# Performance work log

Measured on AMD Instinct MI355X. Metric: run time of the kernel, lower is better.

The kernel has to match this reference:

```python
import jax, jax.numpy as jnp
import numpy as np

N, E, IN, OUT = 50000, 1600000, 64, 64
DIM, K = 2, 5          # pseudo-coordinate dim, kernel size per dim
KP = K ** DIM          # 25 kernel weight matrices
S = 2 ** DIM           # 4 non-zero linear B-spline basis products per edge
# bit pattern per basis product: bits[s, d] in {0,1}
_BITS = np.array([[(s >> d) & 1 for d in range(DIM)] for s in range(S)], dtype=np.int32)
_OFFS = np.array([K ** (DIM - 1 - d) for d in range(DIM)], dtype=np.int32)  # row-major flatten


def setup_inputs() -> dict:
    key = jax.random.key(0)
    ks = jax.random.split(key, 6)
    x = jax.random.normal(ks[0], (N, IN), dtype=jnp.float32)
    edge_index = jax.random.randint(ks[1], (2, E), 0, N)
    pseudo = jax.random.uniform(ks[2], (E, DIM), dtype=jnp.float32)
    bnd = 1.0 / np.sqrt(KP * IN)  # matches uniform(size) init in reset_parameters
    weight = jax.random.uniform(ks[3], (KP, IN, OUT), dtype=jnp.float32, minval=-bnd, maxval=bnd)
    root_weight = jax.random.uniform(ks[4], (IN, OUT), dtype=jnp.float32, minval=-bnd, maxval=bnd)
    bias = jax.random.uniform(ks[5], (OUT,), dtype=jnp.float32, minval=-bnd, maxval=bnd)
    return {"x": x, "edge_index": edge_index, "pseudo": pseudo,
            "weight": weight, "root_weight": root_weight, "bias": bias}


def _basis_and_index(pseudo):
    # open B-spline, degree 1: scale by (K - 1)
    v = pseudo * jnp.asarray(K - 1, pseudo.dtype)          # [E, DIM]
    lo = jnp.floor(v)
    frac = v - lo                                          # [E, DIM]
    lo = lo.astype(jnp.int32)
    bits = jnp.asarray(_BITS)                              # [S, DIM]
    # basis[e, s] = prod_d (frac if bit else 1-frac)
    terms = jnp.where(bits[None].astype(bool), frac[:, None, :], 1.0 - frac[:, None, :])
    basis = jnp.prod(terms, axis=-1)                       # [E, S]
    idx_d = (lo[:, None, :] + bits[None]) % K              # [E, S, DIM]; wrap is harmless (basis=0 there)
    idx = jnp.sum(idx_d * jnp.asarray(_OFFS), axis=-1)     # [E, S] flat weight index in [0, KP)
    return basis, idx


def reference(x, edge_index, pseudo, weight, root_weight, bias):
    row, col = edge_index[0], edge_index[1]                # row = target, col = source
    basis, idx = _basis_and_index(pseudo)                  # [E,S], [E,S]
    x_src = x[col]                                         # [E, IN] gather
    # Accumulate basis-weighted source features per (target node, kernel index),
    # then apply the dense [KP, IN, OUT] weights once (same math, no [E,IN,OUT] blowup).
    acc = jnp.zeros((N * KP, IN), x.dtype)
    for s in range(S):  # S=4, fixed structural loop
        acc = acc + jax.ops.segment_sum(basis[:, s:s + 1] * x_src,
                                        row * KP + idx[:, s], num_segments=N * KP)
    out = jnp.einsum('nki,kio->no', acc.reshape(N, KP, IN), weight)  # [N, OUT]
    deg = jax.ops.segment_sum(jnp.ones((E,), x.dtype), row, num_segments=N)
    out = out / jnp.clip(deg, 1.0)[:, None]                # mean over neighbors (1/N(i))
    return out + x @ root_weight + bias
```

## Files before the change

kernel.cpp:

```cpp
#include <hip/hip_runtime.h>
#include <hip/hip_fp16.h>
#include <hip/hip_bf16.h>


#define NN    50000
#define EE    1600000
#define NPB   16
#define KD    1664
#define ASTB  1672

#define NB    391
#define NSH   4
#define CCAP  1280
#define CSTR  16

#define REC_B 6250
#define XB_B  1563
#define WT_B  104

typedef unsigned short ushort_t;
typedef __attribute__((ext_vector_type(8))) short short8;
typedef __attribute__((ext_vector_type(4))) float f32x4;

static __device__ __forceinline__ ushort_t f2bf(float f) {
  union { float f; unsigned u; } v; v.f = f;
  return (ushort_t)((v.u + 0x7fffu + ((v.u >> 16) & 1u)) >> 16);
}
static __device__ __forceinline__ unsigned pk2bf(float a, float b) {
  __hip_bfloat162 h = __float22bfloat162_rn(make_float2(a, b));
  union { __hip_bfloat162 h; unsigned u; } cv; cv.h = h; return cv.u;
}
union S8 { short8 s; unsigned u[4]; };

__global__ __launch_bounds__(256) void k_prep(
    const int* __restrict__ ei, const float* __restrict__ pseudo,
    int* __restrict__ ccur, uint2* __restrict__ coarse,
    const float* __restrict__ x, ushort_t* __restrict__ xb,
    const float* __restrict__ w, const float* __restrict__ root,
    ushort_t* __restrict__ wt, int useXB) {
  const int b = blockIdx.x;
  const int tid = threadIdx.x;
  if (b < REC_B) {
    int e = b * 256 + tid;
    int row = ei[e], col = ei[EE + e];
    float2 pv = ((const float2*)pseudo)[e];
    float v0 = pv.x * 4.0f, v1 = pv.y * 4.0f;
    unsigned h0 = __half_as_ushort(__float2half(v0));
    unsigned h1 = __half_as_ushort(__float2half(v1));
    int c4 = (row >> 7) * NSH + (tid & (NSH - 1));
    int slot = atomicAdd(&ccur[c4 * CSTR], 1);
    if (slot < CCAP)
      coarse[(size_t)c4 * CCAP + slot] =
          make_uint2((unsigned)col | ((unsigned)(row & 127) << 16), h0 | (h1 << 16));
  } else if (b < REC_B + XB_B) {
    if (!useXB) return;
    int t = (b - REC_B) * 256 + tid;
    if (t < NN * 8) {
      const float4* xp = (const float4*)x + (size_t)t * 2;
      float4 aa = xp[0], bb = xp[1];
      S8 o;
      o.u[0] = pk2bf(aa.x, aa.y); o.u[1] = pk2bf(aa.z, aa.w);
      o.u[2] = pk2bf(bb.x, bb.y); o.u[3] = pk2bf(bb.z, bb.w);
      ((short8*)xb)[t] = o.s;
    }
  } else {
    int t = (b - REC_B - XB_B) * 256 + tid;
    int idx = t * 4;
    if (idx < 64 * KD) {
      int o = idx / KD, k = idx - o * KD;
#pragma unroll
      for (int q = 0; q < 4; ++q) {
        int kk = k + q;
        int kp = kk >> 6, c = kk & 63;
        int fi = 4 * (c & 15) + (c >> 4);
        wt[idx + q] = (kp < 25) ? f2bf(w[(kp * 64 + fi) * 64 + o])
                                : f2bf(root[fi * 64 + o]);
      }
    }
  }
}

__global__ __launch_bounds__(256) void k_sort(
    const int* __restrict__ ccur, const uint2* __restrict__ coarse,
    uint2* __restrict__ recs, uint2* __restrict__ nfo) {
  __shared__ int cnt[128], lpos[128], scn[128], red[256];
  const int c = blockIdx.x, tid = threadIdx.x;
  if (tid < 128) cnt[tid] = 0;
  const int pc = c * NSH;
  int a = 0;
  for (int i = tid; i < pc; i += 256) a += min(ccur[i * CSTR], CCAP);
  red[tid] = a;
  __syncthreads();
  for (int s = 128; s > 0; s >>= 1) { if (tid < s) red[tid] += red[tid + s]; __syncthreads(); }
  const int base = red[0];
  for (int s = 0; s < NSH; ++s) {
    int n = min(ccur[(pc + s) * CSTR], CCAP);
    const uint2* seg = coarse + (size_t)(pc + s) * CCAP;
    for (int i = tid; i < n; i += 256) atomicAdd(&cnt[(seg[i].x >> 16) & 127], 1);
  }
  __syncthreads();
  if (tid < 128) scn[tid] = cnt[tid];
  __syncthreads();
  for (int ofs = 1; ofs < 128; ofs <<= 1) {
    int v = 0;
    if (tid < 128 && tid >= ofs) v = scn[tid - ofs];
    __syncthreads();
    if (tid < 128 && tid >= ofs) scn[tid] += v;
    __syncthreads();
  }
  if (tid < 128) {
    int excl = scn[tid] - cnt[tid];
    lpos[tid] = base + excl;
    int row = c * 128 + tid;
    if (row < NN) nfo[row] = make_uint2((unsigned)(base + excl), (unsigned)cnt[tid]);
  }
  __syncthreads();
  for (int s = 0; s < NSH; ++s) {
    int n = min(ccur[(pc + s) * CSTR], CCAP);
    const uint2* seg = coarse + (size_t)(pc + s) * CCAP;
    for (int i = tid; i < n; i += 256) {
      uint2 r = seg[i];
      int dst = atomicAdd(&lpos[(r.x >> 16) & 127], 1);
      recs[dst] = make_uint2(r.x & 0xFFFFu, r.y);
    }
  }
}

template <bool XBF>
static __device__ __forceinline__ void do_chunk(
    const uint2 (&rq)[8], int kb, int m, int quad, int m15,
    float r0f, float c0f, float r1f, float c1f,
    const ushort_t* __restrict__ xb, const float* __restrict__ x,
    f32x4 (&acc)[2][4]) {
  unsigned cj[8], pj[8];
#pragma unroll
  for (int j = 0; j < 8; ++j) {
    cj[j] = min(rq[j].x, (unsigned)(NN - 1));
    pj[j] = rq[j].y;
  }
  uint2 g[8];
  float gf[4][8];
  if (XBF) {
#pragma unroll
    for (int j = 0; j < 8; ++j)
      g[j] = *(const uint2*)(xb + ((size_t)cj[j] << 6) + (m15 << 2));
  } else {
#pragma unroll
    for (int j = 0; j < 8; ++j) {
      float4 v = *(const float4*)(x + ((size_t)cj[j] << 6) + (m15 << 2));
      gf[0][j] = v.x; gf[1][j] = v.y; gf[2][j] = v.z; gf[3][j] = v.w;
    }
  }
  S8 aT0, aT1, bT[4];
#pragma unroll
  for (int p = 0; p < 4; ++p) {
    float a0[2], a1[2];
#pragma unroll
    for (int q = 0; q < 2; ++q) {
      int j = 2 * p + q;
      unsigned pv = pj[j];
      float v0 = __half2float(__ushort_as_half((ushort_t)(pv & 0xFFFFu)));
      float v1 = __half2float(__ushort_as_half((ushort_t)(pv >> 16)));
      bool ok = (kb + quad * 8 + j) < m;
      float p0 = fmaxf(0.f, 1.f - fabsf(v0 - r0f)) * fmaxf(0.f, 1.f - fabsf(v1 - c0f));
      float p1 = fmaxf(0.f, 1.f - fabsf(v0 - r1f)) * fmaxf(0.f, 1.f - fabsf(v1 - c1f));
      a0[q] = ok ? p0 : 0.0f;
      a1[q] = ok ? p1 : 0.0f;
    }
    aT0.u[p] = pk2bf(a0[0], a0[1]);
    aT1.u[p] = pk2bf(a1[0], a1[1]);
  }
  if (XBF) {
#pragma unroll
    for (int p = 0; p < 4; ++p) {
      bT[0].u[p] = (g[2 * p].x & 0xFFFFu) | (g[2 * p + 1].x << 16);
      bT[1].u[p] = (g[2 * p].x >> 16)     | (g[2 * p + 1].x & 0xFFFF0000u);
      bT[2].u[p] = (g[2 * p].y & 0xFFFFu) | (g[2 * p + 1].y << 16);
      bT[3].u[p] = (g[2 * p].y >> 16)     | (g[2 * p + 1].y & 0xFFFF0000u);
    }
  } else {
#pragma unroll
    for (int p = 0; p < 4; ++p)
#pragma unroll
      for (int t = 0; t < 4; ++t)
        bT[t].u[p] = pk2bf(gf[t][2 * p], gf[t][2 * p + 1]);
  }
  __builtin_amdgcn_s_setprio(1);
#pragma unroll
  for (int t = 0; t < 4; ++t) {
    acc[0][t] = __builtin_amdgcn_mfma_f32_16x16x32_bf16(aT0.s, bT[t].s, acc[0][t], 0, 0, 0);
    acc[1][t] = __builtin_amdgcn_mfma_f32_16x16x32_bf16(aT1.s, bT[t].s, acc[1][t], 0, 0, 0);
  }
  __builtin_amdgcn_s_setprio(0);
}

template <bool XBF>
__global__ __launch_bounds__(512, 4) void k_main(
    const uint2* __restrict__ recs, const uint2* __restrict__ nfo,
    const float* __restrict__ x, const ushort_t* __restrict__ xb,
    const ushort_t* __restrict__ wt, const float* __restrict__ bias,
    float* __restrict__ out) {
  __shared__ ushort_t accS[NPB * ASTB];
  __shared__ float    outp[2 * NPB * 64];
  __shared__ float    sinv[NPB];
  const int tid = threadIdx.x;
  const int lane = tid & 63;
  const int w = tid >> 6;
  const int nb = blockIdx.x * NPB;

  const int m15 = lane & 15, quad = lane >> 4;
  const float r0f = (float)(m15 / 5),        c0f = (float)(m15 % 5);
  const float r1f = (float)((16 + m15) / 5), c1f = (float)((16 + m15) % 5);
  const int fl = 4 * (lane & 15) + (lane >> 4);

#pragma unroll
  for (int nd = 0; nd < 2; ++nd) {
    const int row = (w << 1) + nd;
    const int node = nb + row;
    const uint2 nf = nfo[node];
    const int m = (int)nf.y;
    const float dcf = (float)max(m, 1);
    if (lane == 0) sinv[row] = 1.0f / dcf;
    accS[row * ASTB + 1600 + lane] = f2bf(x[(size_t)node * 64 + fl] * dcf);

    f32x4 acc[2][4];
#pragma unroll
    for (int a = 0; a < 2; ++a)
#pragma unroll
      for (int b = 0; b < 4; ++b) acc[a][b] = (f32x4){0.f, 0.f, 0.f, 0.f};

    const uint2* bket = recs + nf.x;
    for (int e0 = 0; e0 < m; e0 += 32) {
      uint2 rq[8];
#pragma unroll
      for (int j = 0; j < 8; ++j) rq[j] = bket[e0 + quad * 8 + j];
      do_chunk<XBF>(rq, e0, m, quad, m15, r0f, c0f, r1f, c1f, xb, x, acc);
    }

#pragma unroll
    for (int mt = 0; mt < 2; ++mt)
#pragma unroll
      for (int r = 0; r < 4; ++r) {
        int kp = mt * 16 + quad * 4 + r;
        if (kp < 25) {
#pragma unroll
          for (int nt = 0; nt < 4; ++nt)
            accS[row * ASTB + kp * 64 + nt * 16 + m15] = f2bf(acc[mt][nt][r]);
        }
      }
  }
  __syncthreads();

  {
    const int ntile = w & 3, kh = w >> 2;
    const int m2 = lane & 15, quad2 = lane >> 4;
    const int nn2 = ntile * 16 + m2;
    f32x4 d = {0.0f, 0.0f, 0.0f, 0.0f};
    const ushort_t* ab = &accS[m2 * ASTB + kh * 832 + quad2 * 8];
    const ushort_t* wb = &wt[(size_t)nn2 * KD + kh * 832 + quad2 * 8];
    short8 bfs[6];
#pragma unroll
    for (int kk = 0; kk < 6; ++kk) bfs[kk] = *(const short8*)(wb + kk * 32);
#pragma unroll
    for (int kk = 0; kk < 26; ++kk) {
      short8 af = *(const short8*)(ab + kk * 32);
      d = __builtin_amdgcn_mfma_f32_16x16x32_bf16(af, bfs[kk % 6], d, 0, 0, 0);
      if (kk + 6 < 26) bfs[kk % 6] = *(const short8*)(wb + (kk + 6) * 32);
    }
#pragma unroll
    for (int r = 0; r < 4; ++r)
      outp[kh * (NPB * 64) + (quad2 * 4 + r) * 64 + ntile * 16 + m2] = d[r];
  }
  __syncthreads();

  {
#pragma unroll
    for (int h = 0; h < 2; ++h) {
      int i = h * 512 + tid;
      int nl = i >> 6, o = i & 63;
      float conv = outp[i] + outp[NPB * 64 + i];
      out[(size_t)(nb + nl) * 64 + o] = conv * sinv[nl] + bias[o];
    }
  }
}

__global__ void k_sentinel(float* __restrict__ out) {
  int i = blockIdx.x * 256 + threadIdx.x;
  if (i < NN * 64) out[i] = 1000.0f;
}

extern "C" void kernel_launch(void* const* d_in, const int* in_sizes, int n_in,
                              void* d_out, int out_size, void* d_ws, size_t ws_size,
                              hipStream_t stream) {
  const float* x      = (const float*)d_in[0];
  const int*   ei     = (const int*)d_in[1];
  const float* pseudo = (const float*)d_in[2];
  const float* w      = (const float*)d_in[3];
  const float* root   = (const float*)d_in[4];
  const float* bias   = (const float*)d_in[5];
  float* out = (float*)d_out;
  (void)in_sizes; (void)n_in; (void)out_size;

  char* ws = (char*)d_ws;
  size_t off = 0;
  auto alloc = [&](size_t bytes) { size_t r = off; off += (bytes + 511) & ~(size_t)511; return r; };
  ushort_t* wt     = (ushort_t*)(ws + alloc((size_t)64 * KD * 2));
  int*      ccur   = (int*)(ws + alloc((size_t)NB * NSH * CSTR * 4));
  uint2*    nfo    = (uint2*)(ws + alloc((size_t)NN * 8));
  uint2*    recs   = (uint2*)(ws + alloc((size_t)EE * 8));
  uint2*    coarse = (uint2*)(ws + alloc((size_t)NB * NSH * CCAP * 8));
  size_t baseNeed  = off;
  ushort_t* xb     = (ushort_t*)(ws + alloc((size_t)NN * 64 * 2));
  size_t fullNeed  = off;

  if (ws_size < baseNeed) {
    k_sentinel<<<(NN * 64 + 255) / 256, 256, 0, stream>>>(out);
    return;
  }
  const int useXB = (ws_size >= fullNeed) ? 1 : 0;

  hipMemsetAsync(ccur, 0, (size_t)NB * NSH * CSTR * 4, stream);
  k_prep<<<REC_B + XB_B + WT_B, 256, 0, stream>>>(ei, pseudo, ccur, coarse,
                                                  x, xb, w, root, wt, useXB);
  k_sort<<<NB, 256, 0, stream>>>(ccur, coarse, recs, nfo);
  if (useXB)
    k_main<true><<<NN / NPB, 512, 0, stream>>>(recs, nfo, x, xb, wt, bias, out);
  else
    k_main<false><<<NN / NPB, 512, 0, stream>>>(recs, nfo, x, xb, wt, bias, out);
}
```

Baseline: 316.1 us.

## Split each node's feature columns across two waves with 1024-thread blocks

Doubles the block size to 1024 threads so each node's edge aggregation is handled by two waves. Each wave owns half of the 64 output feature columns, gathering 4-byte slices instead of 8-byte ones and issuing half as many MFMAs per chunk. The aim is more parallelism and less register pressure per wave, which helps hide gather latency. The cost is that every edge record and its basis weights are now loaded and computed twice, once per wave, and the dense second stage leaves half the waves idle.

```diff
diff --git a/kernel.cpp b/kernel.cpp
--- a/kernel.cpp
+++ b/kernel.cpp
@@ -128,37 +128,33 @@
 
 template <bool XBF>
 static __device__ __forceinline__ void do_chunk(
-    const uint2 (&rq)[8], int kb, int m, int quad, int m15,
+    const uint2 (&rq)[8], int kb, int m, int quad, int m15, int p,
     float r0f, float c0f, float r1f, float c1f,
     const ushort_t* __restrict__ xb, const float* __restrict__ x,
-    f32x4 (&acc)[2][4]) {
-  unsigned cj[8], pj[8];
-#pragma unroll
-  for (int j = 0; j < 8; ++j) {
-    cj[j] = min(rq[j].x, (unsigned)(NN - 1));
-    pj[j] = rq[j].y;
-  }
-  uint2 g[8];
-  float gf[4][8];
+    f32x4 (&acc)[2][2]) {
+  unsigned g[8];
+  float2 gf[8];
   if (XBF) {
 #pragma unroll
-    for (int j = 0; j < 8; ++j)
-      g[j] = *(const uint2*)(xb + ((size_t)cj[j] << 6) + (m15 << 2));
+    for (int j = 0; j < 8; ++j) {
+      unsigned c = min(rq[j].x, (unsigned)(NN - 1));
+      g[j] = *(const unsigned*)(xb + ((size_t)c << 6) + (m15 << 2) + (p << 1));
+    }
   } else {
 #pragma unroll
     for (int j = 0; j < 8; ++j) {
-      float4 v = *(const float4*)(x + ((size_t)cj[j] << 6) + (m15 << 2));
-      gf[0][j] = v.x; gf[1][j] = v.y; gf[2][j] = v.z; gf[3][j] = v.w;
-    }
-  }
-  S8 aT0, aT1, bT[4];
-#pragma unroll
-  for (int p = 0; p < 4; ++p) {
+      unsigned c = min(rq[j].x, (unsigned)(NN - 1));
+      gf[j] = *(const float2*)(x + ((size_t)c << 6) + (m15 << 2) + (p << 1));
+    }
+  }
+  S8 aT0, aT1, bT[2];
+#pragma unroll
+  for (int pp = 0; pp < 4; ++pp) {
     float a0[2], a1[2];
 #pragma unroll
     for (int q = 0; q < 2; ++q) {
-      int j = 2 * p + q;
-      unsigned pv = pj[j];
+      int j = 2 * pp + q;
+      unsigned pv = rq[j].y;
       float v0 = __half2float(__ushort_as_half((ushort_t)(pv & 0xFFFFu)));
       float v1 = __half2float(__ushort_as_half((ushort_t)(pv >> 16)));
       bool ok = (kb + quad * 8 + j) < m;
@@ -167,27 +163,25 @@
       a0[q] = ok ? p0 : 0.0f;
       a1[q] = ok ? p1 : 0.0f;
     }
-    aT0.u[p] = pk2bf(a0[0], a0[1]);
-    aT1.u[p] = pk2bf(a1[0], a1[1]);
+    aT0.u[pp] = pk2bf(a0[0], a0[1]);
+    aT1.u[pp] = pk2bf(a1[0], a1[1]);
   }
   if (XBF) {
 #pragma unroll
-    for (int p = 0; p < 4; ++p) {
-      bT[0].u[p] = (g[2 * p].x & 0xFFFFu) | (g[2 * p + 1].x << 16);
-      bT[1].u[p] = (g[2 * p].x >> 16)     | (g[2 * p + 1].x & 0xFFFF0000u);
-      bT[2].u[p] = (g[2 * p].y & 0xFFFFu) | (g[2 * p + 1].y << 16);
-      bT[3].u[p] = (g[2 * p].y >> 16)     | (g[2 * p + 1].y & 0xFFFF0000u);
+    for (int pp = 0; pp < 4; ++pp) {
+      bT[0].u[pp] = (g[2 * pp] & 0xFFFFu) | (g[2 * pp + 1] << 16);
+      bT[1].u[pp] = (g[2 * pp] >> 16)     | (g[2 * pp + 1] & 0xFFFF0000u);
     }
   } else {
 #pragma unroll
-    for (int p = 0; p < 4; ++p)
-#pragma unroll
-      for (int t = 0; t < 4; ++t)
-        bT[t].u[p] = pk2bf(gf[t][2 * p], gf[t][2 * p + 1]);
+    for (int pp = 0; pp < 4; ++pp) {
+      bT[0].u[pp] = pk2bf(gf[2 * pp].x, gf[2 * pp + 1].x);
+      bT[1].u[pp] = pk2bf(gf[2 * pp].y, gf[2 * pp + 1].y);
+    }
   }
   __builtin_amdgcn_s_setprio(1);
 #pragma unroll
-  for (int t = 0; t < 4; ++t) {
+  for (int t = 0; t < 2; ++t) {
     acc[0][t] = __builtin_amdgcn_mfma_f32_16x16x32_bf16(aT0.s, bT[t].s, acc[0][t], 0, 0, 0);
     acc[1][t] = __builtin_amdgcn_mfma_f32_16x16x32_bf16(aT1.s, bT[t].s, acc[1][t], 0, 0, 0);
   }
@@ -195,7 +189,7 @@
 }
 
 template <bool XBF>
-__global__ __launch_bounds__(512, 4) void k_main(
+__global__ __launch_bounds__(1024, 8) void k_main(
     const uint2* __restrict__ recs, const uint2* __restrict__ nfo,
     const float* __restrict__ x, const ushort_t* __restrict__ xb,
     const ushort_t* __restrict__ wt, const float* __restrict__ bias,
@@ -206,35 +200,40 @@
   const int tid = threadIdx.x;
   const int lane = tid & 63;
   const int w = tid >> 6;
+  const int p = w & 1;
+  const int np = w >> 1;
   const int nb = blockIdx.x * NPB;
 
   const int m15 = lane & 15, quad = lane >> 4;
   const float r0f = (float)(m15 / 5),        c0f = (float)(m15 % 5);
   const float r1f = (float)((16 + m15) / 5), c1f = (float)((16 + m15) % 5);
-  const int fl = 4 * (lane & 15) + (lane >> 4);
 
 #pragma unroll
   for (int nd = 0; nd < 2; ++nd) {
-    const int row = (w << 1) + nd;
+    const int row = (np << 1) + nd;
     const int node = nb + row;
     const uint2 nf = nfo[node];
     const int m = (int)nf.y;
     const float dcf = (float)max(m, 1);
-    if (lane == 0) sinv[row] = 1.0f / dcf;
-    accS[row * ASTB + 1600 + lane] = f2bf(x[(size_t)node * 64 + fl] * dcf);
-
-    f32x4 acc[2][4];
+    if (p == 0 && lane == 0) sinv[row] = 1.0f / dcf;
+    if (lane < 32) {
+      int c = (p << 5) + lane;
+      int fi = 4 * (c & 15) + (c >> 4);
+      accS[row * ASTB + 1600 + c] = f2bf(x[(size_t)node * 64 + fi] * dcf);
+    }
+
+    f32x4 acc[2][2];
 #pragma unroll
     for (int a = 0; a < 2; ++a)
 #pragma unroll
-      for (int b = 0; b < 4; ++b) acc[a][b] = (f32x4){0.f, 0.f, 0.f, 0.f};
+      for (int b = 0; b < 2; ++b) acc[a][b] = (f32x4){0.f, 0.f, 0.f, 0.f};
 
     const uint2* bket = recs + nf.x;
     for (int e0 = 0; e0 < m; e0 += 32) {
       uint2 rq[8];
 #pragma unroll
       for (int j = 0; j < 8; ++j) rq[j] = bket[e0 + quad * 8 + j];
-      do_chunk<XBF>(rq, e0, m, quad, m15, r0f, c0f, r1f, c1f, xb, x, acc);
+      do_chunk<XBF>(rq, e0, m, quad, m15, p, r0f, c0f, r1f, c1f, xb, x, acc);
     }
 
 #pragma unroll
@@ -244,14 +243,15 @@
         int kp = mt * 16 + quad * 4 + r;
         if (kp < 25) {
 #pragma unroll
-          for (int nt = 0; nt < 4; ++nt)
-            accS[row * ASTB + kp * 64 + nt * 16 + m15] = f2bf(acc[mt][nt][r]);
+          for (int t = 0; t < 2; ++t)
+            accS[row * ASTB + kp * 64 + ((p << 1) + t) * 16 + m15] =
+                f2bf(acc[mt][t][r]);
         }
       }
   }
   __syncthreads();
 
-  {
+  if (w < 8) {
     const int ntile = w & 3, kh = w >> 2;
     const int m2 = lane & 15, quad2 = lane >> 4;
     const int nn2 = ntile * 16 + m2;
@@ -274,13 +274,9 @@
   __syncthreads();
 
   {
-#pragma unroll
-    for (int h = 0; h < 2; ++h) {
-      int i = h * 512 + tid;
-      int nl = i >> 6, o = i & 63;
-      float conv = outp[i] + outp[NPB * 64 + i];
-      out[(size_t)(nb + nl) * 64 + o] = conv * sinv[nl] + bias[o];
-    }
+    int nl = tid >> 6, o = tid & 63;
+    float conv = outp[tid] + outp[NPB * 64 + tid];
+    out[(size_t)(nb + nl) * 64 + o] = conv * sinv[nl] + bias[o];
   }
 }
 
@@ -324,7 +320,7 @@
                                                   x, xb, w, root, wt, useXB);
   k_sort<<<NB, 256, 0, stream>>>(ccur, coarse, recs, nfo);
   if (useXB)
-    k_main<true><<<NN / NPB, 512, 0, stream>>>(recs, nfo, x, xb, wt, bias, out);
+    k_main<true><<<NN / NPB, 1024, 0, stream>>>(recs, nfo, x, xb, wt, bias, out);
   else
-    k_main<false><<<NN / NPB, 512, 0, stream>>>(recs, nfo, x, xb, wt, bias, out);
-}
+    k_main<false><<<NN / NPB, 1024, 0, stream>>>(recs, nfo, x, xb, wt, bias, out);
+}
```

Result: slower. 344.7 us (+9.1%).

## Preload edge records per node via lane loads and shuffles, issue two gather chunks ahead

Applied to the files above, without the earlier changes.

Each wave now loads the first 64 edge records of both of its nodes up front, one record per lane, and hands them to the gather step with warp shuffles instead of per-lane scalar loads. For the first two 32-edge chunks it issues all feature gathers before doing any MFMA compute, which raises memory-level parallelism and hides gather latency. Nodes with more than 64 edges fall back to the old per-chunk loop. Out-of-range lanes are padded with half-precision infinity coordinates so their basis weights become zero. The cost is more live registers, which may reduce occupancy.

```diff
diff --git a/kernel.cpp b/kernel.cpp
--- a/kernel.cpp
+++ b/kernel.cpp
@@ -126,6 +126,52 @@
   }
 }
 
+static __device__ __forceinline__ void issue_chunk(
+    unsigned wx, unsigned wy, int base, int quad, int m15,
+    const ushort_t* __restrict__ xb, unsigned (&pj)[8], uint2 (&g)[8]) {
+#pragma unroll
+  for (int j = 0; j < 8; ++j) {
+    int e = base + quad * 8 + j;
+    unsigned cjv = (unsigned)__shfl((int)wx, e);
+    pj[j] = (unsigned)__shfl((int)wy, e);
+    g[j] = *(const uint2*)(xb + ((size_t)cjv << 6) + (m15 << 2));
+  }
+}
+
+static __device__ __forceinline__ void compute_chunk(
+    const unsigned (&pj)[8], const uint2 (&g)[8],
+    float r0f, float c0f, float r1f, float c1f, f32x4 (&acc)[2][4]) {
+  S8 aT0, aT1, bT[4];
+#pragma unroll
+  for (int p = 0; p < 4; ++p) {
+    float a0[2], a1[2];
+#pragma unroll
+    for (int q = 0; q < 2; ++q) {
+      unsigned pv = pj[2 * p + q];
+      float v0 = __half2float(__ushort_as_half((ushort_t)(pv & 0xFFFFu)));
+      float v1 = __half2float(__ushort_as_half((ushort_t)(pv >> 16)));
+      a0[q] = fmaxf(0.f, 1.f - fabsf(v0 - r0f)) * fmaxf(0.f, 1.f - fabsf(v1 - c0f));
+      a1[q] = fmaxf(0.f, 1.f - fabsf(v0 - r1f)) * fmaxf(0.f, 1.f - fabsf(v1 - c1f));
+    }
+    aT0.u[p] = pk2bf(a0[0], a0[1]);
+    aT1.u[p] = pk2bf(a1[0], a1[1]);
+  }
+#pragma unroll
+  for (int p = 0; p < 4; ++p) {
+    bT[0].u[p] = (g[2 * p].x & 0xFFFFu) | (g[2 * p + 1].x << 16);
+    bT[1].u[p] = (g[2 * p].x >> 16)     | (g[2 * p + 1].x & 0xFFFF0000u);
+    bT[2].u[p] = (g[2 * p].y & 0xFFFFu) | (g[2 * p + 1].y << 16);
+    bT[3].u[p] = (g[2 * p].y >> 16)     | (g[2 * p + 1].y & 0xFFFF0000u);
+  }
+  __builtin_amdgcn_s_setprio(1);
+#pragma unroll
+  for (int t = 0; t < 4; ++t) {
+    acc[0][t] = __builtin_amdgcn_mfma_f32_16x16x32_bf16(aT0.s, bT[t].s, acc[0][t], 0, 0, 0);
+    acc[1][t] = __builtin_amdgcn_mfma_f32_16x16x32_bf16(aT1.s, bT[t].s, acc[1][t], 0, 0, 0);
+  }
+  __builtin_amdgcn_s_setprio(0);
+}
+
 template <bool XBF>
 static __device__ __forceinline__ void do_chunk(
     const uint2 (&rq)[8], int kb, int m, int quad, int m15,
@@ -185,13 +231,26 @@
       for (int t = 0; t < 4; ++t)
         bT[t].u[p] = pk2bf(gf[t][2 * p], gf[t][2 * p + 1]);
   }
-  __builtin_amdgcn_s_setprio(1);
 #pragma unroll
   for (int t = 0; t < 4; ++t) {
     acc[0][t] = __builtin_amdgcn_mfma_f32_16x16x32_bf16(aT0.s, bT[t].s, acc[0][t], 0, 0, 0);
     acc[1][t] = __builtin_amdgcn_mfma_f32_16x16x32_bf16(aT1.s, bT[t].s, acc[1][t], 0, 0, 0);
   }
-  __builtin_amdgcn_s_setprio(0);
+}
+
+static __device__ __forceinline__ void spill_acc(
+    ushort_t* accS, int row, int quad, int m15, const f32x4 (&acc)[2][4]) {
+#pragma unroll
+  for (int mt = 0; mt < 2; ++mt)
+#pragma unroll
+    for (int r = 0; r < 4; ++r) {
+      int kp = mt * 16 + quad * 4 + r;
+      if (kp < 25) {
+#pragma unroll
+        for (int nt = 0; nt < 4; ++nt)
+          accS[row * ASTB + kp * 64 + nt * 16 + m15] = f2bf(acc[mt][nt][r]);
+      }
+    }
 }
 
 template <bool XBF>
@@ -211,43 +270,91 @@
   const int m15 = lane & 15, quad = lane >> 4;
   const float r0f = (float)(m15 / 5),        c0f = (float)(m15 % 5);
   const float r1f = (float)((16 + m15) / 5), c1f = (float)((16 + m15) % 5);
-  const int fl = 4 * (lane & 15) + (lane >> 4);
-
-#pragma unroll
-  for (int nd = 0; nd < 2; ++nd) {
-    const int row = (w << 1) + nd;
-    const int node = nb + row;
-    const uint2 nf = nfo[node];
-    const int m = (int)nf.y;
-    const float dcf = (float)max(m, 1);
-    if (lane == 0) sinv[row] = 1.0f / dcf;
-    accS[row * ASTB + 1600 + lane] = f2bf(x[(size_t)node * 64 + fl] * dcf);
-
-    f32x4 acc[2][4];
+  const int fl = 4 * m15 + quad;
+
+  const int rowA = w << 1, rowB = rowA + 1;
+  const int nodeA = nb + rowA, nodeB = nb + rowB;
+
+  const uint2 nfA = nfo[nodeA], nfB = nfo[nodeB];
+  const float rxA = x[(size_t)nodeA * 64 + fl];
+  const float rxB = x[(size_t)nodeB * 64 + fl];
+  const int mA = (int)nfA.y, mB = (int)nfB.y;
+  unsigned wAx = 0u, wAy = 0x7C007C00u, wBx = 0u, wBy = 0x7C007C00u;
+  if (lane < mA) { uint2 rr = recs[nfA.x + lane]; wAx = rr.x; wAy = rr.y; }
+  if (lane < mB) { uint2 rr = recs[nfB.x + lane]; wBx = rr.x; wBy = rr.y; }
+
+  const float dcfA = (float)max(mA, 1), dcfB = (float)max(mB, 1);
+  if (lane == 0) { sinv[rowA] = 1.0f / dcfA; sinv[rowB] = 1.0f / dcfB; }
+  accS[rowA * ASTB + 1600 + lane] = f2bf(rxA * dcfA);
+  accS[rowB * ASTB + 1600 + lane] = f2bf(rxB * dcfB);
+
+  f32x4 acc[2][4];
+#pragma unroll
+  for (int a = 0; a < 2; ++a)
+#pragma unroll
+    for (int b = 0; b < 4; ++b) acc[a][b] = (f32x4){0.f, 0.f, 0.f, 0.f};
+
+  if (XBF) {
+    if (mA > 32) {
+      unsigned pj0[8], pj1[8]; uint2 g0[8], g1[8];
+      issue_chunk(wAx, wAy, 0,  quad, m15, xb, pj0, g0);
+      issue_chunk(wAx, wAy, 32, quad, m15, xb, pj1, g1);
+      compute_chunk(pj0, g0, r0f, c0f, r1f, c1f, acc);
+      compute_chunk(pj1, g1, r0f, c0f, r1f, c1f, acc);
+    } else if (mA > 0) {
+      unsigned pj0[8]; uint2 g0[8];
+      issue_chunk(wAx, wAy, 0, quad, m15, xb, pj0, g0);
+      compute_chunk(pj0, g0, r0f, c0f, r1f, c1f, acc);
+    }
+    for (int e0 = 64; e0 < mA; e0 += 32) {
+      uint2 rq[8];
+#pragma unroll
+      for (int j = 0; j < 8; ++j) rq[j] = recs[nfA.x + e0 + quad * 8 + j];
+      do_chunk<true>(rq, e0, mA, quad, m15, r0f, c0f, r1f, c1f, xb, x, acc);
+    }
+    spill_acc(accS, rowA, quad, m15, acc);
+
 #pragma unroll
     for (int a = 0; a < 2; ++a)
 #pragma unroll
       for (int b = 0; b < 4; ++b) acc[a][b] = (f32x4){0.f, 0.f, 0.f, 0.f};
-
-    const uint2* bket = recs + nf.x;
-    for (int e0 = 0; e0 < m; e0 += 32) {
+    if (mB > 32) {
+      unsigned pj0[8], pj1[8]; uint2 g0[8], g1[8];
+      issue_chunk(wBx, wBy, 0,  quad, m15, xb, pj0, g0);
+      issue_chunk(wBx, wBy, 32, quad, m15, xb, pj1, g1);
+      compute_chunk(pj0, g0, r0f, c0f, r1f, c1f, acc);
+      compute_chunk(pj1, g1, r0f, c0f, r1f, c1f, acc);
+    } else if (mB > 0) {
+      unsigned pj0[8]; uint2 g0[8];
+      issue_chunk(wBx, wBy, 0, quad, m15, xb, pj0, g0);
+      compute_chunk(pj0, g0, r0f, c0f, r1f, c1f, acc);
+    }
+    for (int e0 = 64; e0 < mB; e0 += 32) {
       uint2 rq[8];
 #pragma unroll
-      for (int j = 0; j < 8; ++j) rq[j] = bket[e0 + quad * 8 + j];
-      do_chunk<XBF>(rq, e0, m, quad, m15, r0f, c0f, r1f, c1f, xb, x, acc);
-    }
-
-#pragma unroll
-    for (int mt = 0; mt < 2; ++mt)
-#pragma unroll
-      for (int r = 0; r < 4; ++r) {
-        int kp = mt * 16 + quad * 4 + r;
-        if (kp < 25) {
-#pragma unroll
-          for (int nt = 0; nt < 4; ++nt)
-            accS[row * ASTB + kp * 64 + nt * 16 + m15] = f2bf(acc[mt][nt][r]);
-        }
-      }
+      for (int j = 0; j < 8; ++j) rq[j] = recs[nfB.x + e0 + quad * 8 + j];
+      do_chunk<true>(rq, e0, mB, quad, m15, r0f, c0f, r1f, c1f, xb, x, acc);
+    }
+    spill_acc(accS, rowB, quad, m15, acc);
+  } else {
+    for (int e0 = 0; e0 < mA; e0 += 32) {
+      uint2 rq[8];
+#pragma unroll
+      for (int j = 0; j < 8; ++j) rq[j] = recs[nfA.x + e0 + quad * 8 + j];
+      do_chunk<false>(rq, e0, mA, quad, m15, r0f, c0f, r1f, c1f, xb, x, acc);
+    }
+    spill_acc(accS, rowA, quad, m15, acc);
+#pragma unroll
+    for (int a = 0; a < 2; ++a)
+#pragma unroll
+      for (int b = 0; b < 4; ++b) acc[a][b] = (f32x4){0.f, 0.f, 0.f, 0.f};
+    for (int e0 = 0; e0 < mB; e0 += 32) {
+      uint2 rq[8];
+#pragma unroll
+      for (int j = 0; j < 8; ++j) rq[j] = recs[nfB.x + e0 + quad * 8 + j];
+      do_chunk<false>(rq, e0, mB, quad, m15, r0f, c0f, r1f, c1f, xb, x, acc);
+    }
+    spill_acc(accS, rowB, quad, m15, acc);
   }
   __syncthreads();
 
```

Result: faster. 303.3 us (-4.0%).
